# Kernel tuning notes

Measured on AMD Instinct MI355X. Metric: run time of the kernel, lower is better.

## Reference

```python
import jax, jax.numpy as jnp
import numpy as np

N_HEADS = 8
D_HEAD = 64
INNER = N_HEADS * D_HEAD  # 512
D_X = 512
D_CTX = 768

def setup_inputs() -> dict:
    key = jax.random.key(0)
    ks = jax.random.split(key, 7)
    x = jax.random.normal(ks[0], (4, 4096, D_X), dtype=jnp.float32)
    context = jax.random.normal(ks[1], (4, 1024, D_CTX), dtype=jnp.float32)
    # Glorot-ish scaled params
    Wq = jax.random.normal(ks[2], (D_X, INNER), dtype=jnp.float32) / np.sqrt(D_X)
    Wk = jax.random.normal(ks[3], (D_CTX, INNER), dtype=jnp.float32) / np.sqrt(D_CTX)
    Wv = jax.random.normal(ks[4], (D_CTX, INNER), dtype=jnp.float32) / np.sqrt(D_CTX)
    Wo = jax.random.normal(ks[5], (INNER, INNER), dtype=jnp.float32) / np.sqrt(INNER)
    bo = jnp.zeros((INNER,), dtype=jnp.float32)
    return {"x": x, "context": context, "Wq": Wq, "Wk": Wk, "Wv": Wv, "Wo": Wo, "bo": bo}

def reference(x, context, Wq, Wk, Wv, Wo, bo):
    B, Nq, _ = x.shape
    Nc = context.shape[1]
    scale = D_HEAD ** -0.5
    # QKV projections (no bias), reshape to heads: b s (h d) -> b h s d
    q = (x @ Wq).reshape(B, Nq, N_HEADS, D_HEAD).transpose(0, 2, 1, 3)
    k = (context @ Wk).reshape(B, Nc, N_HEADS, D_HEAD).transpose(0, 2, 1, 3)
    v = (context @ Wv).reshape(B, Nc, N_HEADS, D_HEAD).transpose(0, 2, 1, 3)
    # scores: [B, H, Nq, Nc]
    score = jnp.einsum('bhqd,bhkd->bhqk', q, k) * scale
    weights = jax.nn.softmax(score, axis=-1)
    attn = jnp.einsum('bhqk,bhkd->bhqd', weights, v)
    out = attn.transpose(0, 2, 1, 3).reshape(B, Nq, INNER)
    return out @ Wo + bo
```

## Files before the change

### kernel.cpp

```cpp
#include <hip/hip_runtime.h>
#include <math.h>

typedef __attribute__((ext_vector_type(8))) short s8v;
typedef __attribute__((ext_vector_type(4))) float f4v;
typedef unsigned short u16;
typedef unsigned int u32;

constexpr int Bsz = 4, NQ = 4096, NC = 1024, NH = 8, DH = 64, DI = 512, DC = 768;

__device__ __forceinline__ u16 f2bf(float f) {
  union { float f; u32 u; } v; v.f = f;
  u32 r = v.u + 0x7fff + ((v.u >> 16) & 1);
  return (u16)(r >> 16);
}

__device__ __forceinline__ u32 pack2(float a, float b) {
  union { float f; u32 u; } ua, ub; ua.f = a; ub.f = b;
#if __has_builtin(__builtin_amdgcn_perm)
  return __builtin_amdgcn_perm(ub.u + 0x8000u, ua.u + 0x8000u, 0x07060302u);
#else
  return ((ub.u + 0x8000u) & 0xffff0000u) | ((ua.u + 0x8000u) >> 16);
#endif
}

__device__ __forceinline__ u32 cvtpk(float a, float b) {
  u32 r;
  asm("v_cvt_pk_bf16_f32 %0, %1, %2" : "=v"(r) : "v"(a), "v"(b));
  return r;
}

#if __has_builtin(__builtin_amdgcn_exp2f)
#define EXP2(x) __builtin_amdgcn_exp2f(x)
#else
#define EXP2(x) exp2f(x)
#endif

__device__ __forceinline__ void g2l16(const void* g, void* l) {
  __builtin_amdgcn_global_load_lds((const __attribute__((address_space(1))) u32*)g,
                                   (__attribute__((address_space(3))) u32*)l, 16, 0, 0);
}

__global__ __launch_bounds__(256) void prep(const float* __restrict__ x, const float* __restrict__ ctx,
                                            const float* __restrict__ Wq, const float* __restrict__ Wk,
                                            const float* __restrict__ Wv, const float* __restrict__ Wo,
                                            u16* __restrict__ xb, u16* __restrict__ cb,
                                            u16* __restrict__ wqT, u16* __restrict__ wkvT,
                                            u16* __restrict__ woT) {
  int bx = blockIdx.x;
  if (bx < 11264) {
    const int NX4 = Bsz * NQ * DI / 4;
    const int NC4 = Bsz * NC * DC / 4;
    int i = bx * 256 + threadIdx.x;
    float4 v; u16* dst; int j;
    if (i < NX4) { v = ((const float4*)x)[i]; dst = xb; j = i; }
    else { j = i - NX4; if (j >= NC4) return; v = ((const float4*)ctx)[j]; dst = cb; }
    ushort4 o; o.x = f2bf(v.x); o.y = f2bf(v.y); o.z = f2bf(v.z); o.w = f2bf(v.w);
    ((ushort4*)dst)[j] = o;
    return;
  }
  int idx = bx - 11264;
  int z = idx / 96, rem = idx % 96, kx = rem % 12, ny = rem / 12;
  const float* src; u16* dst; int K; const int N = 512;
  if (z == 0)      { src = Wq; dst = wqT;              K = 512; }
  else if (z == 1) { src = Wk; dst = wkvT;             K = 768; }
  else if (z == 2) { src = Wv; dst = wkvT + 512 * 768; K = 768; }
  else             { src = Wo; dst = woT;              K = 512; }
  int k0 = kx * 64, n0 = ny * 64;
  if (k0 >= K) return;
  __shared__ u16 t[64][65];
  int tid = threadIdx.x, jr = tid & 63, ir = tid >> 6;
  for (int it = 0; it < 16; ++it) { int i = it * 4 + ir; t[i][jr] = f2bf(src[(size_t)(k0 + i) * N + n0 + jr]); }
  __syncthreads();
  for (int it = 0; it < 16; ++it) { int i = it * 4 + ir; dst[(size_t)(n0 + i) * K + k0 + jr] = t[jr][i]; }
}

template <int MODE>
__device__ __forceinline__ void gemm_body(const u16* __restrict__ A, const u16* __restrict__ Bt,
                                          void* __restrict__ C0, void* __restrict__ C1,
                                          const float* __restrict__ bias, int N, int K,
                                          float oscale, int nbx, int mby,
                                          u16* Al, u16* Bl) {
  int mb = mby * 128, nb = nbx * 128;
  int tid = threadIdx.x, lane = tid & 63, quad = lane >> 4, l16 = lane & 15, wave = tid >> 6;
  int wm = (wave >> 1) * 64, wn = (wave & 1) * 64;
  f4v acc[4][4];
  #pragma unroll
  for (int i = 0; i < 4; i++)
    #pragma unroll
    for (int j = 0; j < 4; j++) acc[i][j] = (f4v){0.f, 0.f, 0.f, 0.f};

  int r0 = tid >> 2, c0 = (tid & 3) * 8;
  const u16* Ap0 = A + (size_t)(mb + r0) * K + c0;
  const u16* Ap1 = A + (size_t)(mb + r0 + 64) * K + c0;
  const u16* Bp0 = Bt + (size_t)(nb + r0) * K + c0;
  const u16* Bp1 = Bt + (size_t)(nb + r0 + 64) * K + c0;

#define GSTAGE(k0, buf) do { \
    u16* al_ = Al + (buf) * 4096; u16* bl_ = Bl + (buf) * 4096; \
    g2l16(Ap0 + (k0), al_ + tid * 8); \
    g2l16(Ap1 + (k0), al_ + (tid + 256) * 8); \
    g2l16(Bp0 + (k0), bl_ + tid * 8); \
    g2l16(Bp1 + (k0), bl_ + (tid + 256) * 8); } while (0)

  GSTAGE(0, 0);
  int nk = K >> 5;
  for (int t = 0; t < nk; ++t) {
    __syncthreads();
    if (t + 1 < nk) GSTAGE((t + 1) * 32, (t + 1) & 1);
    const u16* al = Al + (t & 1) * 4096;
    const u16* bl = Bl + (t & 1) * 4096;
    s8v af[4], bfr[4];
    #pragma unroll
    for (int i = 0; i < 4; i++) af[i] = *(const s8v*)(al + (wm + i * 16 + l16) * 32 + quad * 8);
    #pragma unroll
    for (int j = 0; j < 4; j++) bfr[j] = *(const s8v*)(bl + (wn + j * 16 + l16) * 32 + quad * 8);
    #pragma unroll
    for (int i = 0; i < 4; i++)
      #pragma unroll
      for (int j = 0; j < 4; j++)
        acc[i][j] = __builtin_amdgcn_mfma_f32_16x16x32_bf16(af[i], bfr[j], acc[i][j], 0, 0, 0);
  }
#undef GSTAGE
  #pragma unroll
  for (int i = 0; i < 4; i++) {
    int rbase = mb + wm + i * 16 + quad * 4;
    #pragma unroll
    for (int j = 0; j < 4; j++) {
      int col = nb + wn + j * 16 + l16;
      if (MODE == 0) {
        u16* Cb = (u16*)C0;
        #pragma unroll
        for (int r = 0; r < 4; r++) Cb[(size_t)(rbase + r) * N + col] = f2bf(acc[i][j][r] * oscale);
      } else if (MODE == 1) {
        float* Cf = (float*)C0;
        #pragma unroll
        for (int r = 0; r < 4; r++) Cf[(size_t)(rbase + r) * N + col] = acc[i][j][r] + bias[col];
      } else {
        if (col < 512) {
          u16* Kb = (u16*)C0;
          #pragma unroll
          for (int r = 0; r < 4; r++) Kb[(size_t)(rbase + r) * 512 + col] = f2bf(acc[i][j][r]);
        } else {
          u16* Vt = (u16*)C1;
          int hd = col - 512, h = hd >> 6, d = hd & 63;
          int bb = rbase >> 10, tl = rbase & 1023;
          int tbase = tl & ~63, a0 = tl & 63;
          int pb = (a0 & 32) + ((a0 & 15) >> 2) * 8 + (((a0 >> 4) & 1) << 2);
          uint2 ov;
          ov.x = pack2(acc[i][j][0], acc[i][j][1]);
          ov.y = pack2(acc[i][j][2], acc[i][j][3]);
          *(uint2*)(Vt + ((size_t)(bb * NH + h) * DH + d) * NC + tbase + pb) = ov;
        }
      }
    }
  }
}

__global__ __launch_bounds__(256, 3) void proj_all(const u16* __restrict__ xb, const u16* __restrict__ cb,
                                                   const u16* __restrict__ wqT, const u16* __restrict__ wkvT,
                                                   u16* __restrict__ Qb, u16* __restrict__ Kb,
                                                   u16* __restrict__ Vtb, float qscale) {
  __shared__ alignas(16) u16 Al[2][128][32];
  __shared__ alignas(16) u16 Bl[2][128][32];
  int bx = blockIdx.x;
  if (bx < 512) {
    gemm_body<0>(xb, wqT, Qb, nullptr, nullptr, 512, 512, qscale, bx & 3, bx >> 2,
                 (u16*)Al, (u16*)Bl);
  } else {
    int bi = bx - 512;
    gemm_body<2>(cb, wkvT, Kb, Vtb, nullptr, 1024, 768, 1.0f, bi & 7, bi >> 3,
                 (u16*)Al, (u16*)Bl);
  }
}

__global__ __launch_bounds__(256, 2) void outproj(const u16* __restrict__ Ob, const u16* __restrict__ woT,
                                                  float* __restrict__ out, const float* __restrict__ bo) {
  __shared__ alignas(16) u16 Al[2][128][32];
  __shared__ alignas(16) u16 Bl[2][128][32];
  gemm_body<1>(Ob, woT, out, nullptr, bo, 512, 512, 1.0f, blockIdx.x, blockIdx.y,
               (u16*)Al, (u16*)Bl);
}

__global__ __launch_bounds__(256, 4) void attn(const u16* __restrict__ Q, const u16* __restrict__ Kb,
                                               const u16* __restrict__ Vt, u16* __restrict__ O) {
  __shared__ alignas(16) u16 Kl[2][64][64];
  __shared__ alignas(16) u16 Vl[2][64][64];
  int qt = blockIdx.x, h = blockIdx.y, b = blockIdx.z;
  int tid = threadIdx.x, wave = tid >> 6, lane = tid & 63, quad = lane >> 4, l16 = lane & 15;
  int q0 = qt * 128 + wave * 32;
  int x7 = l16 & 7;

  int kr = tid >> 3, kc = (tid & 7) ^ (kr & 7);
  const u16* kg = Kb + ((size_t)b * NC + kr) * 512 + h * DH + kc * 8;
  const u16* vg = Vt + ((size_t)(b * NH + h) * DH + kr) * NC + kc * 8;

#define ASTAGE(kt, buf) do { \
    const u16* kg_ = kg + (size_t)(kt) * 64 * 512; \
    const u16* vg_ = vg + (kt) * 64; \
    u16* kl_ = (u16*)Kl + (buf) * 4096; u16* vl_ = (u16*)Vl + (buf) * 4096; \
    g2l16(kg_,            kl_ + tid * 8); \
    g2l16(kg_ + 32 * 512, kl_ + (tid + 256) * 8); \
    g2l16(vg_,            vl_ + tid * 8); \
    g2l16(vg_ + 32 * NC,  vl_ + (tid + 256) * 8); } while (0)

  s8v aq[2][2];
  {
    const u16* Qp = Q + ((size_t)b * NQ + q0 + l16) * DI + h * DH + quad * 8;
    #pragma unroll
    for (int n = 0; n < 2; n++) {
      aq[n][0] = *(const s8v*)(Qp + (size_t)n * 16 * DI);
      aq[n][1] = *(const s8v*)(Qp + (size_t)n * 16 * DI + 32);
    }
  }
  s8v vones;
  #pragma unroll
  for (int i = 0; i < 8; i++) vones[i] = (short)0x3F80;

  f4v oacc[4][2];
  f4v lacc[2];
  #pragma unroll
  for (int d = 0; d < 4; d++)
    #pragma unroll
    for (int n = 0; n < 2; n++) oacc[d][n] = (f4v){0.f, 0.f, 0.f, 0.f};
  #pragma unroll
  for (int n = 0; n < 2; n++) lacc[n] = (f4v){0.f, 0.f, 0.f, 0.f};

  ASTAGE(0, 0);
  for (int kt = 0; kt < NC / 64; ++kt) {
    int buf = kt & 1;
    __syncthreads();
    if (kt + 1 < NC / 64) ASTAGE(kt + 1, buf ^ 1);
    const u16* kb = (const u16*)Kl + buf * 4096;
    const u16* vb = (const u16*)Vl + buf * 4096;

    f4v S0[2][2], S1[2][2];
    #pragma unroll
    for (int mi = 0; mi < 2; mi++)
      #pragma unroll
      for (int n = 0; n < 2; n++) { S0[mi][n] = (f4v){0.f,0.f,0.f,0.f}; S1[mi][n] = (f4v){0.f,0.f,0.f,0.f}; }
    __builtin_amdgcn_s_setprio(1);
    #pragma unroll
    for (int cd = 0; cd < 2; cd++) {
      int ch = ((4 * cd + quad) ^ x7) * 8;
      s8v k00 = *(const s8v*)(kb + (l16     ) * 64 + ch);
      s8v k01 = *(const s8v*)(kb + (l16 + 16) * 64 + ch);
      #pragma unroll
      for (int n = 0; n < 2; n++) {
        S0[0][n] = __builtin_amdgcn_mfma_f32_16x16x32_bf16(k00, aq[n][cd], S0[0][n], 0, 0, 0);
        S0[1][n] = __builtin_amdgcn_mfma_f32_16x16x32_bf16(k01, aq[n][cd], S0[1][n], 0, 0, 0);
      }
      s8v k10 = *(const s8v*)(kb + (l16 + 32) * 64 + ch);
      s8v k11 = *(const s8v*)(kb + (l16 + 48) * 64 + ch);
      #pragma unroll
      for (int n = 0; n < 2; n++) {
        S1[0][n] = __builtin_amdgcn_mfma_f32_16x16x32_bf16(k10, aq[n][cd], S1[0][n], 0, 0, 0);
        S1[1][n] = __builtin_amdgcn_mfma_f32_16x16x32_bf16(k11, aq[n][cd], S1[1][n], 0, 0, 0);
      }
    }
    __builtin_amdgcn_s_setprio(0);

    s8v pf0[2];
    #pragma unroll
    for (int n = 0; n < 2; n++) {
      float p00 = EXP2(S0[0][n][0]), p01 = EXP2(S0[0][n][1]), p02 = EXP2(S0[0][n][2]), p03 = EXP2(S0[0][n][3]);
      float p10 = EXP2(S0[1][n][0]), p11 = EXP2(S0[1][n][1]), p12 = EXP2(S0[1][n][2]), p13 = EXP2(S0[1][n][3]);
      union { u32 d[4]; s8v v; } u;
      u.d[0] = cvtpk(p00, p01); u.d[1] = cvtpk(p02, p03);
      u.d[2] = cvtpk(p10, p11); u.d[3] = cvtpk(p12, p13);
      pf0[n] = u.v;
    }
    __builtin_amdgcn_s_setprio(1);
    #pragma unroll
    for (int n = 0; n < 2; n++)
      lacc[n] = __builtin_amdgcn_mfma_f32_16x16x32_bf16(vones, pf0[n], lacc[n], 0, 0, 0);
    #pragma unroll
    for (int d = 0; d < 4; d++) {
      int ch = (quad ^ x7) * 8;
      s8v vf = *(const s8v*)(vb + (d * 16 + l16) * 64 + ch);
      #pragma unroll
      for (int n = 0; n < 2; n++)
        oacc[d][n] = __builtin_amdgcn_mfma_f32_16x16x32_bf16(vf, pf0[n], oacc[d][n], 0, 0, 0);
    }
    __builtin_amdgcn_s_setprio(0);

    s8v pf1[2];
    #pragma unroll
    for (int n = 0; n < 2; n++) {
      float p00 = EXP2(S1[0][n][0]), p01 = EXP2(S1[0][n][1]), p02 = EXP2(S1[0][n][2]), p03 = EXP2(S1[0][n][3]);
      float p10 = EXP2(S1[1][n][0]), p11 = EXP2(S1[1][n][1]), p12 = EXP2(S1[1][n][2]), p13 = EXP2(S1[1][n][3]);
      union { u32 d[4]; s8v v; } u;
      u.d[0] = cvtpk(p00, p01); u.d[1] = cvtpk(p02, p03);
      u.d[2] = cvtpk(p10, p11); u.d[3] = cvtpk(p12, p13);
      pf1[n] = u.v;
    }
    __builtin_amdgcn_s_setprio(1);
    #pragma unroll
    for (int n = 0; n < 2; n++)
      lacc[n] = __builtin_amdgcn_mfma_f32_16x16x32_bf16(vones, pf1[n], lacc[n], 0, 0, 0);
    #pragma unroll
    for (int d = 0; d < 4; d++) {
      int ch = ((4 + quad) ^ x7) * 8;
      s8v vf = *(const s8v*)(vb + (d * 16 + l16) * 64 + ch);
      #pragma unroll
      for (int n = 0; n < 2; n++)
        oacc[d][n] = __builtin_amdgcn_mfma_f32_16x16x32_bf16(vf, pf1[n], oacc[d][n], 0, 0, 0);
    }
    __builtin_amdgcn_s_setprio(0);
  }
#undef ASTAGE

  float inv[2];
  #pragma unroll
  for (int n = 0; n < 2; n++) inv[n] = 1.0f / lacc[n][0];

  #pragma unroll
  for (int d = 0; d < 4; d++)
    #pragma unroll
    for (int n = 0; n < 2; n++) {
      int q = q0 + n * 16 + l16;
      uint2 ov;
      ov.x = cvtpk(oacc[d][n][0] * inv[n], oacc[d][n][1] * inv[n]);
      ov.y = cvtpk(oacc[d][n][2] * inv[n], oacc[d][n][3] * inv[n]);
      *(uint2*)(O + ((size_t)b * NQ + q) * DI + h * DH + d * 16 + quad * 4) = ov;
    }
}

extern "C" void kernel_launch(void* const* d_in, const int* in_sizes, int n_in,
                              void* d_out, int out_size, void* d_ws, size_t ws_size,
                              hipStream_t stream) {
  const float* x   = (const float*)d_in[0];
  const float* ctx = (const float*)d_in[1];
  const float* Wq  = (const float*)d_in[2];
  const float* Wk  = (const float*)d_in[3];
  const float* Wv  = (const float*)d_in[4];
  const float* Wo  = (const float*)d_in[5];
  const float* bo  = (const float*)d_in[6];
  float* out = (float*)d_out;

  u16* w    = (u16*)d_ws;
  u16* xb   = w;
  u16* cb   = xb   + 8388608;
  u16* wqT  = cb   + 3145728;
  u16* wkvT = wqT  + 262144;
  u16* woT  = wkvT + 786432;
  u16* Qb   = woT  + 262144;
  u16* Kbuf = Qb   + 8388608;
  u16* Vtb  = Kbuf + 2097152;
  u16* Ob   = Vtb  + 2097152;

  const float qscale = 0.125f * 1.44269504f;

  prep<<<11648, 256, 0, stream>>>(x, ctx, Wq, Wk, Wv, Wo, xb, cb, wqT, wkvT, woT);
  proj_all<<<768, 256, 0, stream>>>(xb, cb, wqT, wkvT, Qb, Kbuf, Vtb, qscale);
  attn<<<dim3(32, 8, 4), 256, 0, stream>>>(Qb, Kbuf, Vtb, Ob);
  outproj<<<dim3(4, 128), 256, 0, stream>>>(Ob, woT, out, bo);
}
```

Before: 188.3 us.

## Fuse fp32-to-bf16 activation conversion into projection GEMM loads with swizzled LDS

After: 194.3 us. 3.2% more time.

```diff
diff --git a/kernel.cpp b/kernel.cpp
--- a/kernel.cpp
+++ b/kernel.cpp
@@ -40,25 +40,11 @@
                                    (__attribute__((address_space(3))) u32*)l, 16, 0, 0);
 }
 
-__global__ __launch_bounds__(256) void prep(const float* __restrict__ x, const float* __restrict__ ctx,
-                                            const float* __restrict__ Wq, const float* __restrict__ Wk,
+__global__ __launch_bounds__(256) void prep(const float* __restrict__ Wq, const float* __restrict__ Wk,
                                             const float* __restrict__ Wv, const float* __restrict__ Wo,
-                                            u16* __restrict__ xb, u16* __restrict__ cb,
                                             u16* __restrict__ wqT, u16* __restrict__ wkvT,
                                             u16* __restrict__ woT) {
-  int bx = blockIdx.x;
-  if (bx < 11264) {
-    const int NX4 = Bsz * NQ * DI / 4;
-    const int NC4 = Bsz * NC * DC / 4;
-    int i = bx * 256 + threadIdx.x;
-    float4 v; u16* dst; int j;
-    if (i < NX4) { v = ((const float4*)x)[i]; dst = xb; j = i; }
-    else { j = i - NX4; if (j >= NC4) return; v = ((const float4*)ctx)[j]; dst = cb; }
-    ushort4 o; o.x = f2bf(v.x); o.y = f2bf(v.y); o.z = f2bf(v.z); o.w = f2bf(v.w);
-    ((ushort4*)dst)[j] = o;
-    return;
-  }
-  int idx = bx - 11264;
+  int idx = blockIdx.x;
   int z = idx / 96, rem = idx % 96, kx = rem % 12, ny = rem / 12;
   const float* src; u16* dst; int K; const int N = 512;
   if (z == 0)      { src = Wq; dst = wqT;              K = 512; }
@@ -74,8 +60,8 @@
   for (int it = 0; it < 16; ++it) { int i = it * 4 + ir; dst[(size_t)(n0 + i) * K + k0 + jr] = t[jr][i]; }
 }
 
-template <int MODE>
-__device__ __forceinline__ void gemm_body(const u16* __restrict__ A, const u16* __restrict__ Bt,
+template <int MODE, bool F32A>
+__device__ __forceinline__ void gemm_body(const void* __restrict__ Av, const u16* __restrict__ Bt,
                                           void* __restrict__ C0, void* __restrict__ C1,
                                           const float* __restrict__ bias, int N, int K,
                                           float oscale, int nbx, int mby,
@@ -89,38 +75,67 @@
     #pragma unroll
     for (int j = 0; j < 4; j++) acc[i][j] = (f4v){0.f, 0.f, 0.f, 0.f};
 
-  int r0 = tid >> 2, c0 = (tid & 3) * 8;
-  const u16* Ap0 = A + (size_t)(mb + r0) * K + c0;
-  const u16* Ap1 = A + (size_t)(mb + r0 + 64) * K + c0;
-  const u16* Bp0 = Bt + (size_t)(nb + r0) * K + c0;
-  const u16* Bp1 = Bt + (size_t)(nb + r0 + 64) * K + c0;
-
-#define GSTAGE(k0, buf) do { \
-    u16* al_ = Al + (buf) * 4096; u16* bl_ = Bl + (buf) * 4096; \
-    g2l16(Ap0 + (k0), al_ + tid * 8); \
-    g2l16(Ap1 + (k0), al_ + (tid + 256) * 8); \
-    g2l16(Bp0 + (k0), bl_ + tid * 8); \
-    g2l16(Bp1 + (k0), bl_ + (tid + 256) * 8); } while (0)
-
-  GSTAGE(0, 0);
+  int r0 = tid >> 2;
+  int cs = ((tid & 3) ^ ((r0 >> 1) & 3)) * 8;
+  int lin = tid * 8;
+  const u16* Bp0 = Bt + (size_t)(nb + r0) * K + cs;
+  const u16* Bp1 = Bt + (size_t)(nb + r0 + 64) * K + cs;
+  const float* Af0 = nullptr; const float* Af1 = nullptr;
+  const u16* Ap0 = nullptr; const u16* Ap1 = nullptr;
+  if constexpr (F32A) {
+    Af0 = (const float*)Av + (size_t)(mb + r0) * K + cs;
+    Af1 = Af0 + (size_t)64 * K;
+  } else {
+    Ap0 = (const u16*)Av + (size_t)(mb + r0) * K + cs;
+    Ap1 = Ap0 + (size_t)64 * K;
+  }
+  float4 a00, a01, a10, a11;
+
+#define BSTAGE(k0, buf) do { u16* bl_ = Bl + (buf) * 4096; \
+    g2l16(Bp0 + (k0), bl_ + lin); g2l16(Bp1 + (k0), bl_ + lin + 2048); } while (0)
+#define ASTAGE_G(k0, buf) do { u16* al_ = Al + (buf) * 4096; \
+    g2l16(Ap0 + (k0), al_ + lin); g2l16(Ap1 + (k0), al_ + lin + 2048); } while (0)
+#define ALOAD(k0) do { \
+    a00 = *(const float4*)(Af0 + (k0)); a01 = *(const float4*)(Af0 + (k0) + 4); \
+    a10 = *(const float4*)(Af1 + (k0)); a11 = *(const float4*)(Af1 + (k0) + 4); } while (0)
+#define AWRITE(buf) do { u16* al_ = Al + (buf) * 4096; \
+    union { u32 d[4]; s8v v; } ua, ub; \
+    ua.d[0] = cvtpk(a00.x, a00.y); ua.d[1] = cvtpk(a00.z, a00.w); \
+    ua.d[2] = cvtpk(a01.x, a01.y); ua.d[3] = cvtpk(a01.z, a01.w); \
+    ub.d[0] = cvtpk(a10.x, a10.y); ub.d[1] = cvtpk(a10.z, a10.w); \
+    ub.d[2] = cvtpk(a11.x, a11.y); ub.d[3] = cvtpk(a11.z, a11.w); \
+    *(s8v*)(al_ + lin) = ua.v; *(s8v*)(al_ + lin + 2048) = ub.v; } while (0)
+
+  if constexpr (F32A) { ALOAD(0); BSTAGE(0, 0); AWRITE(0); }
+  else { ASTAGE_G(0, 0); BSTAGE(0, 0); }
+
   int nk = K >> 5;
+  int swq8 = (quad ^ ((l16 >> 1) & 3)) * 8;
   for (int t = 0; t < nk; ++t) {
     __syncthreads();
-    if (t + 1 < nk) GSTAGE((t + 1) * 32, (t + 1) & 1);
+    int nxt = (t + 1) * 32, nbuf = (t + 1) & 1;
+    if (t + 1 < nk) {
+      if constexpr (F32A) ALOAD(nxt); else ASTAGE_G(nxt, nbuf);
+      BSTAGE(nxt, nbuf);
+    }
     const u16* al = Al + (t & 1) * 4096;
     const u16* bl = Bl + (t & 1) * 4096;
     s8v af[4], bfr[4];
     #pragma unroll
-    for (int i = 0; i < 4; i++) af[i] = *(const s8v*)(al + (wm + i * 16 + l16) * 32 + quad * 8);
-    #pragma unroll
-    for (int j = 0; j < 4; j++) bfr[j] = *(const s8v*)(bl + (wn + j * 16 + l16) * 32 + quad * 8);
+    for (int i = 0; i < 4; i++) af[i] = *(const s8v*)(al + (wm + i * 16 + l16) * 32 + swq8);
+    #pragma unroll
+    for (int j = 0; j < 4; j++) bfr[j] = *(const s8v*)(bl + (wn + j * 16 + l16) * 32 + swq8);
     #pragma unroll
     for (int i = 0; i < 4; i++)
       #pragma unroll
       for (int j = 0; j < 4; j++)
         acc[i][j] = __builtin_amdgcn_mfma_f32_16x16x32_bf16(af[i], bfr[j], acc[i][j], 0, 0, 0);
-  }
-#undef GSTAGE
+    if constexpr (F32A) { if (t + 1 < nk) AWRITE(nbuf); }
+  }
+#undef BSTAGE
+#undef ASTAGE_G
+#undef ALOAD
+#undef AWRITE
   #pragma unroll
   for (int i = 0; i < 4; i++) {
     int rbase = mb + wm + i * 16 + quad * 4;
@@ -156,20 +171,20 @@
   }
 }
 
-__global__ __launch_bounds__(256, 3) void proj_all(const u16* __restrict__ xb, const u16* __restrict__ cb,
+__global__ __launch_bounds__(256, 3) void proj_all(const float* __restrict__ x, const float* __restrict__ ctx,
                                                    const u16* __restrict__ wqT, const u16* __restrict__ wkvT,
                                                    u16* __restrict__ Qb, u16* __restrict__ Kb,
                                                    u16* __restrict__ Vtb, float qscale) {
   __shared__ alignas(16) u16 Al[2][128][32];
   __shared__ alignas(16) u16 Bl[2][128][32];
   int bx = blockIdx.x;
-  if (bx < 512) {
-    gemm_body<0>(xb, wqT, Qb, nullptr, nullptr, 512, 512, qscale, bx & 3, bx >> 2,
-                 (u16*)Al, (u16*)Bl);
+  if (bx < 256) {
+    gemm_body<2, true>(ctx, wkvT, Kb, Vtb, nullptr, 1024, 768, 1.0f, bx & 7, bx >> 3,
+                       (u16*)Al, (u16*)Bl);
   } else {
-    int bi = bx - 512;
-    gemm_body<2>(cb, wkvT, Kb, Vtb, nullptr, 1024, 768, 1.0f, bi & 7, bi >> 3,
-                 (u16*)Al, (u16*)Bl);
+    int bi = bx - 256;
+    gemm_body<0, true>(x, wqT, Qb, nullptr, nullptr, 512, 512, qscale, bi & 3, bi >> 2,
+                       (u16*)Al, (u16*)Bl);
   }
 }
 
@@ -177,8 +192,8 @@
                                                   float* __restrict__ out, const float* __restrict__ bo) {
   __shared__ alignas(16) u16 Al[2][128][32];
   __shared__ alignas(16) u16 Bl[2][128][32];
-  gemm_body<1>(Ob, woT, out, nullptr, bo, 512, 512, 1.0f, blockIdx.x, blockIdx.y,
-               (u16*)Al, (u16*)Bl);
+  gemm_body<1, false>(Ob, woT, out, nullptr, bo, 512, 512, 1.0f, blockIdx.x, blockIdx.y,
+                      (u16*)Al, (u16*)Bl);
 }
 
 __global__ __launch_bounds__(256, 4) void attn(const u16* __restrict__ Q, const u16* __restrict__ Kb,
@@ -338,9 +353,7 @@
   float* out = (float*)d_out;
 
   u16* w    = (u16*)d_ws;
-  u16* xb   = w;
-  u16* cb   = xb   + 8388608;
-  u16* wqT  = cb   + 3145728;
+  u16* wqT  = w;
   u16* wkvT = wqT  + 262144;
   u16* woT  = wkvT + 786432;
   u16* Qb   = woT  + 262144;
@@ -350,8 +363,8 @@
 
   const float qscale = 0.125f * 1.44269504f;
 
-  prep<<<11648, 256, 0, stream>>>(x, ctx, Wq, Wk, Wv, Wo, xb, cb, wqT, wkvT, woT);
-  proj_all<<<768, 256, 0, stream>>>(xb, cb, wqT, wkvT, Qb, Kbuf, Vtb, qscale);
+  prep<<<384, 256, 0, stream>>>(Wq, Wk, Wv, Wo, wqT, wkvT, woT);
+  proj_all<<<768, 256, 0, stream>>>(x, ctx, wqT, wkvT, Qb, Kbuf, Vtb, qscale);
   attn<<<dim3(32, 8, 4), 256, 0, stream>>>(Qb, Kbuf, Vtb, Ob);
   outproj<<<dim3(4, 128), 256, 0, stream>>>(Ob, woT, out, bo);
 }
```

## Rewrite projection GEMMs with 8-wave 128x256 tiles and triple-buffered LDS pipeline

Applied to the files above, without the earlier changes.

Result: faster. 179.2 us (-4.9%).

```diff
diff --git a/kernel.cpp b/kernel.cpp
--- a/kernel.cpp
+++ b/kernel.cpp
@@ -75,52 +75,91 @@
 }
 
 template <int MODE>
-__device__ __forceinline__ void gemm_body(const u16* __restrict__ A, const u16* __restrict__ Bt,
-                                          void* __restrict__ C0, void* __restrict__ C1,
-                                          const float* __restrict__ bias, int N, int K,
-                                          float oscale, int nbx, int mby,
-                                          u16* Al, u16* Bl) {
-  int mb = mby * 128, nb = nbx * 128;
-  int tid = threadIdx.x, lane = tid & 63, quad = lane >> 4, l16 = lane & 15, wave = tid >> 6;
-  int wm = (wave >> 1) * 64, wn = (wave & 1) * 64;
+__device__ __forceinline__ void gemm8p(const u16* __restrict__ A, const u16* __restrict__ Bt,
+                                       void* __restrict__ C0, void* __restrict__ C1,
+                                       const float* __restrict__ bias, int N, int K,
+                                       float oscale, int nbx, int mby,
+                                       u16* Ash, u16* Bsh) {
+  int tid = threadIdx.x;
+  int lane = tid & 63, quad = lane >> 4, l16 = lane & 15, wave = tid >> 6;
+  int wm = (wave >> 2) * 64, wn = (wave & 3) * 64;
+  int mb = mby * 128, nb = nbx * 256;
+  int x7 = l16 & 7;
   f4v acc[4][4];
   #pragma unroll
   for (int i = 0; i < 4; i++)
     #pragma unroll
     for (int j = 0; j < 4; j++) acc[i][j] = (f4v){0.f, 0.f, 0.f, 0.f};
 
-  int r0 = tid >> 2, c0 = (tid & 3) * 8;
-  const u16* Ap0 = A + (size_t)(mb + r0) * K + c0;
-  const u16* Ap1 = A + (size_t)(mb + r0 + 64) * K + c0;
-  const u16* Bp0 = Bt + (size_t)(nb + r0) * K + c0;
-  const u16* Bp1 = Bt + (size_t)(nb + r0 + 64) * K + c0;
-
-#define GSTAGE(k0, buf) do { \
-    u16* al_ = Al + (buf) * 4096; u16* bl_ = Bl + (buf) * 4096; \
-    g2l16(Ap0 + (k0), al_ + tid * 8); \
-    g2l16(Ap1 + (k0), al_ + (tid + 256) * 8); \
-    g2l16(Bp0 + (k0), bl_ + tid * 8); \
-    g2l16(Bp1 + (k0), bl_ + (tid + 256) * 8); } while (0)
-
-  GSTAGE(0, 0);
-  int nk = K >> 5;
-  for (int t = 0; t < nk; ++t) {
-    __syncthreads();
-    if (t + 1 < nk) GSTAGE((t + 1) * 32, (t + 1) & 1);
-    const u16* al = Al + (t & 1) * 4096;
-    const u16* bl = Bl + (t & 1) * 4096;
-    s8v af[4], bfr[4];
-    #pragma unroll
-    for (int i = 0; i < 4; i++) af[i] = *(const s8v*)(al + (wm + i * 16 + l16) * 32 + quad * 8);
-    #pragma unroll
-    for (int j = 0; j < 4; j++) bfr[j] = *(const s8v*)(bl + (wn + j * 16 + l16) * 32 + quad * 8);
-    #pragma unroll
-    for (int i = 0; i < 4; i++)
-      #pragma unroll
-      for (int j = 0; j < 4; j++)
-        acc[i][j] = __builtin_amdgcn_mfma_f32_16x16x32_bf16(af[i], bfr[j], acc[i][j], 0, 0, 0);
-  }
-#undef GSTAGE
+  int srow = tid >> 3;
+  int sc = ((tid & 7) ^ (srow & 7)) * 8;
+  const u16* Ap0 = A  + (size_t)(mb + srow) * K + sc;
+  const u16* Bq0 = Bt + (size_t)(nb + srow) * K + sc;
+  int lin = tid * 8;
+
+#define SA(ts, dst) do { const u16* s_ = Ap0 + (size_t)(ts) * 64; \
+    g2l16(s_, (dst) + lin); g2l16(s_ + (size_t)64 * K, (dst) + 4096 + lin); } while (0)
+#define SB0(ts, dst) do { const u16* s_ = Bq0 + (size_t)(ts) * 64; \
+    g2l16(s_, (dst) + lin); g2l16(s_ + (size_t)64 * K, (dst) + 4096 + lin); } while (0)
+#define SB1(ts, dst) do { const u16* s_ = Bq0 + (size_t)(ts) * 64 + (size_t)128 * K; \
+    g2l16(s_, (dst) + 8192 + lin); g2l16(s_ + (size_t)64 * K, (dst) + 12288 + lin); } while (0)
+
+  int ak0 = ((0 + quad) ^ x7) * 8;
+  int ak1 = ((4 + quad) ^ x7) * 8;
+
+  s8v bfr[4];
+#define PHASE(ABUF, BBUF, AKK, IP, LOADB, WAITN, ...) do { \
+    if (LOADB) { \
+      bfr[0] = *(const s8v*)((BBUF) + (wn +  0 + l16) * 64 + (AKK)); \
+      bfr[1] = *(const s8v*)((BBUF) + (wn + 16 + l16) * 64 + (AKK)); \
+      bfr[2] = *(const s8v*)((BBUF) + (wn + 32 + l16) * 64 + (AKK)); \
+      bfr[3] = *(const s8v*)((BBUF) + (wn + 48 + l16) * 64 + (AKK)); \
+    } \
+    s8v af0 = *(const s8v*)((ABUF) + (wm + (IP) * 32 + l16) * 64 + (AKK)); \
+    s8v af1 = *(const s8v*)((ABUF) + (wm + (IP) * 32 + 16 + l16) * 64 + (AKK)); \
+    __VA_ARGS__; \
+    { int wv_ = (WAITN); \
+      if (wv_ == 6) asm volatile("s_waitcnt vmcnt(6)" ::: "memory"); \
+      else if (wv_ == 0) asm volatile("s_waitcnt vmcnt(0)" ::: "memory"); } \
+    asm volatile("" ::: "memory"); __builtin_amdgcn_s_barrier(); asm volatile("" ::: "memory"); \
+    __builtin_amdgcn_s_setprio(1); \
+    _Pragma("unroll") \
+    for (int j = 0; j < 4; j++) { \
+      acc[(IP)*2][j]   = __builtin_amdgcn_mfma_f32_16x16x32_bf16(af0, bfr[j], acc[(IP)*2][j],   0, 0, 0); \
+      acc[(IP)*2+1][j] = __builtin_amdgcn_mfma_f32_16x16x32_bf16(af1, bfr[j], acc[(IP)*2+1][j], 0, 0, 0); \
+    } \
+    __builtin_amdgcn_s_setprio(0); \
+    asm volatile("" ::: "memory"); __builtin_amdgcn_s_barrier(); asm volatile("" ::: "memory"); \
+  } while (0)
+
+  u16 *A0 = Ash, *A1 = Ash + 8192, *A2 = Ash + 16384;
+  u16 *B0 = Bsh, *B1 = Bsh + 16384, *B2 = Bsh + 32768;
+
+  SA(0, A0); SB0(0, B0); SB1(0, B0);
+  SA(1, A1); SB0(1, B1); SB1(1, B1);
+  asm volatile("s_waitcnt vmcnt(6)" ::: "memory");
+  __builtin_amdgcn_s_barrier();
+  asm volatile("" ::: "memory");
+
+  int nkt = K >> 6;
+  for (int t2 = 0; t2 < nkt; t2 += 2) {
+    bool more = (t2 + 2 < nkt);
+    PHASE(A0, B0, ak0, 0, true,  -1, if (more) SA(t2 + 2, A2));
+    PHASE(A0, B0, ak0, 1, false, -1, if (more) SB0(t2 + 2, B2));
+    PHASE(A0, B0, ak1, 0, true,  -1, if (more) SB1(t2 + 2, B2));
+    PHASE(A0, B0, ak1, 1, false, (more ? 6 : 0), );
+    PHASE(A1, B1, ak0, 0, true,  -1, if (more) SA(t2 + 3, A0));
+    PHASE(A1, B1, ak0, 1, false, -1, if (more) SB0(t2 + 3, B0));
+    PHASE(A1, B1, ak1, 0, true,  -1, if (more) SB1(t2 + 3, B0));
+    PHASE(A1, B1, ak1, 1, false, (more ? 6 : -1), );
+    u16* tA = A0; A0 = A2; A2 = A1; A1 = tA;
+    u16* tB = B0; B0 = B2; B2 = B1; B1 = tB;
+  }
+#undef PHASE
+#undef SA
+#undef SB0
+#undef SB1
+
   #pragma unroll
   for (int i = 0; i < 4; i++) {
     int rbase = mb + wm + i * 16 + quad * 4;
@@ -156,29 +195,30 @@
   }
 }
 
-__global__ __launch_bounds__(256, 3) void proj_all(const u16* __restrict__ xb, const u16* __restrict__ cb,
+__global__ __launch_bounds__(512, 2) void proj_all(const u16* __restrict__ xb, const u16* __restrict__ cb,
                                                    const u16* __restrict__ wqT, const u16* __restrict__ wkvT,
                                                    u16* __restrict__ Qb, u16* __restrict__ Kb,
                                                    u16* __restrict__ Vtb, float qscale) {
-  __shared__ alignas(16) u16 Al[2][128][32];
-  __shared__ alignas(16) u16 Bl[2][128][32];
+  __shared__ alignas(16) u16 Ash[3 * 8192];
+  __shared__ alignas(16) u16 Bsh[3 * 16384];
   int bx = blockIdx.x;
-  if (bx < 512) {
-    gemm_body<0>(xb, wqT, Qb, nullptr, nullptr, 512, 512, qscale, bx & 3, bx >> 2,
-                 (u16*)Al, (u16*)Bl);
+  if (bx < 128) {
+    int bi = (bx & 7) * 16 + (bx >> 3);
+    gemm8p<2>(cb, wkvT, Kb, Vtb, nullptr, 1024, 768, 1.0f, bi & 3, bi >> 2, Ash, Bsh);
   } else {
-    int bi = bx - 512;
-    gemm_body<2>(cb, wkvT, Kb, Vtb, nullptr, 1024, 768, 1.0f, bi & 7, bi >> 3,
-                 (u16*)Al, (u16*)Bl);
-  }
-}
-
-__global__ __launch_bounds__(256, 2) void outproj(const u16* __restrict__ Ob, const u16* __restrict__ woT,
+    int bq = bx - 128;
+    int bi = (bq & 7) * 32 + (bq >> 3);
+    gemm8p<0>(xb, wqT, Qb, nullptr, nullptr, 512, 512, qscale, bi & 1, bi >> 1, Ash, Bsh);
+  }
+}
+
+__global__ __launch_bounds__(512, 2) void outproj(const u16* __restrict__ Ob, const u16* __restrict__ woT,
                                                   float* __restrict__ out, const float* __restrict__ bo) {
-  __shared__ alignas(16) u16 Al[2][128][32];
-  __shared__ alignas(16) u16 Bl[2][128][32];
-  gemm_body<1>(Ob, woT, out, nullptr, bo, 512, 512, 1.0f, blockIdx.x, blockIdx.y,
-               (u16*)Al, (u16*)Bl);
+  __shared__ alignas(16) u16 Ash[3 * 8192];
+  __shared__ alignas(16) u16 Bsh[3 * 16384];
+  int bx = blockIdx.x;
+  int bi = (bx & 7) * 32 + (bx >> 3);
+  gemm8p<1>(Ob, woT, out, nullptr, bo, 512, 512, 1.0f, bi & 1, bi >> 1, Ash, Bsh);
 }
 
 __global__ __launch_bounds__(256, 4) void attn(const u16* __restrict__ Q, const u16* __restrict__ Kb,
@@ -351,7 +391,7 @@
   const float qscale = 0.125f * 1.44269504f;
 
   prep<<<11648, 256, 0, stream>>>(x, ctx, Wq, Wk, Wv, Wo, xb, cb, wqT, wkvT, woT);
-  proj_all<<<768, 256, 0, stream>>>(xb, cb, wqT, wkvT, Qb, Kbuf, Vtb, qscale);
+  proj_all<<<384, 512, 0, stream>>>(xb, cb, wqT, wkvT, Qb, Kbuf, Vtb, qscale);
   attn<<<dim3(32, 8, 4), 256, 0, stream>>>(Qb, Kbuf, Vtb, Ob);
-  outproj<<<dim3(4, 128), 256, 0, stream>>>(Ob, woT, out, bo);
-}
+  outproj<<<256, 512, 0, stream>>>(Ob, woT, out, bo);
+}
```
